# Optimization experiments

Measured on AMD Instinct MI355X. Metric: run time of the kernel, lower is better.

## Reference

```python
import jax, jax.numpy as jnp
import numpy as np

E = 23   # unique_experts_num
K = 3    # act_experts_num
D = 1024 # in_features
H = 768  # hidden_features (0.75 * dim, per MOEBlock mlp_ratio)


def setup_inputs() -> dict:
    key = jax.random.key(0)
    ks = jax.random.split(key, 12)
    s_in = 1.0 / np.sqrt(D)
    s_hid = 1.0 / np.sqrt(H)
    x = jax.random.normal(ks[0], (4, 1024, D), dtype=jnp.float32)
    gate_W = jax.random.normal(ks[1], (D, E), dtype=jnp.float32) * s_in
    gate_b = jnp.zeros((E,), jnp.float32)
    bias = jnp.zeros((E,), jnp.float32)  # registered buffer, init to zeros
    W1 = jax.random.normal(ks[2], (E, D, H), dtype=jnp.float32) * s_in
    b1 = jnp.zeros((E, H), jnp.float32)
    W2 = jax.random.normal(ks[3], (E, H, D), dtype=jnp.float32) * s_hid
    b2 = jnp.zeros((E, D), jnp.float32)
    sW1 = jax.random.normal(ks[4], (D, H), dtype=jnp.float32) * s_in
    sb1 = jnp.zeros((H,), jnp.float32)
    sW2 = jax.random.normal(ks[5], (H, D), dtype=jnp.float32) * s_hid
    sb2 = jnp.zeros((D,), jnp.float32)
    return {"x": x, "gate_W": gate_W, "gate_b": gate_b, "bias": bias,
            "W1": W1, "b1": b1, "W2": W2, "b2": b2,
            "sW1": sW1, "sb1": sb1, "sW2": sW2, "sb2": sb2}


def reference(x, gate_W, gate_b, bias, W1, b1, W2, b2, sW1, sb1, sW2, sb2):
    o_shape = x.shape
    xt = x.reshape(-1, o_shape[-1])          # [T, D]
    T = xt.shape[0]

    # gating: sigmoid gate, top-k indices chosen on (gate + bias), weights gathered from gate
    gate = jax.nn.sigmoid(xt @ gate_W + gate_b)            # [T, E]
    _, top_idx = jax.lax.top_k(gate + bias, K)             # [T, K]
    top_w = jnp.take_along_axis(gate, top_idx, axis=-1)    # [T, K]
    top_w = top_w / jnp.sum(top_w, axis=-1, keepdims=True)

    # combine matrix: C[t, e] = normalized gate weight if e in top-k of token t else 0
    C = jnp.zeros((T, E), xt.dtype).at[jnp.arange(T)[:, None], top_idx].set(top_w)

    # all-expert dense compute (math-equivalent to dispatch/compute/combine)
    h = jax.nn.gelu(jnp.einsum('td,edh->eth', xt, W1) + b1[:, None, :], approximate=False)
    y = jnp.einsum('eth,ehd->etd', h, W2) + b2[:, None, :]  # [E, T, D]
    moe_out = jnp.einsum('etd,te->td', y, C)                # weighted combine

    # shared expert applied to every token
    shared = jax.nn.gelu(xt @ sW1 + sb1, approximate=False) @ sW2 + sb2
    out = shared + moe_out

    # aux load-balance loss
    gate_norm = gate / jnp.sum(gate, axis=-1, keepdims=True)
    P = jnp.mean(gate_norm, axis=0)                          # [E]
    counts = jnp.sum(jax.nn.one_hot(top_idx, E, dtype=jnp.float32), axis=(0, 1))  # [E]
    F = E * counts / (K * T)
    aux_loss = jnp.sum(P * F)

    return out.reshape(o_shape), aux_loss, counts.astype(jnp.int32)
```

## Files before the change

### kernel.cpp

```cpp
#include <hip/hip_runtime.h>
#include <math.h>

#define TT 4096
#define DD 1024
#define HH 768
#define NE 23
#define NG 24
#define BM 128
#define BN 128
#define BK 64
#define MAXT 160
#define KB1 16
#define KB2 12
#define NY1 6
#define NY2 8
#define NWG1 (MAXT*NY1)
#define NWG2 (MAXT*NY2)
#define GATE_BLKS 1024
#define CVT1_BLKS 1152
#define CVT_TOT   2304

#define WS_CURS   0
#define WS_OFFS   576
#define WS_TOTAL  640
#define WS_T2E    672
#define WS_T2A    832
#define WS_TOKE   1024
#define WS_TOKW   13312
#define WS_LTOK   25600
#define WS_LW     41984
#define WS_PPART  58368
#define WS_CPART  81920
#define WS_SIDX   106496
#define XB_OFF  ((size_t)524288)
#define H_OFF   ((size_t)8912896)
#define W1B_OFF ((size_t)34078720)
#define W2B_OFF ((size_t)71827456)

typedef short bf16x8 __attribute__((ext_vector_type(8)));
typedef float f32x4 __attribute__((ext_vector_type(4)));

#define S_BARRIER() asm volatile("s_barrier" ::: "memory")
#define WAIT_VM0()  asm volatile("s_waitcnt vmcnt(0)" ::: "memory")

__device__ inline unsigned short bfr(float f) {
    unsigned u = __float_as_uint(f);
    u += 0x7fffu + ((u >> 16) & 1u);
    return (unsigned short)(u >> 16);
}
__device__ inline unsigned bfr2(float lo, float hi) {
    return (unsigned)bfr(lo) | ((unsigned)bfr(hi) << 16);
}
__device__ inline float b2f(unsigned short u) {
    return __uint_as_float((unsigned)u << 16);
}

__device__ __forceinline__ void gl_lds16(const void* g, void* l) {
    __builtin_amdgcn_global_load_lds(
        (const __attribute__((address_space(1))) unsigned int*)g,
        (__attribute__((address_space(3))) unsigned int*)l, 16, 0, 0);
}

__device__ __forceinline__ void cvt_tile(
    const float* __restrict__ src, unsigned short* __restrict__ dst,
    int N, int KBt, int e, int kb0, int n0, void* smem, int tid)
{
    unsigned (*Ls)[32][65] = (unsigned (*)[32][65])smem;
    const int c = (tid & 15) * 4, r2l = tid >> 4;
    #pragma unroll
    for (int t = 0; t < 2; t++) {
        const float* tsrc = src + (size_t)(kb0 + t) * 64 * N + n0;
        #pragma unroll
        for (int pass = 0; pass < 2; pass++) {
            int row2 = pass * 16 + r2l;
            float4 v0 = *(const float4*)(tsrc + (size_t)(2 * row2) * N + c);
            float4 v1 = *(const float4*)(tsrc + (size_t)(2 * row2 + 1) * N + c);
            uint4 o;
            o.x = bfr2(v0.x, v1.x); o.y = bfr2(v0.y, v1.y);
            o.z = bfr2(v0.z, v1.z); o.w = bfr2(v0.w, v1.w);
            *(uint4*)&Ls[t][row2][c] = o;
        }
    }
    __syncthreads();
    #pragma unroll
    for (int t = 0; t < 2; t++) {
        unsigned short* dbase = dst + ((size_t)(e * KBt + kb0 + t) * N + n0) * 64;
        #pragma unroll
        for (int half = 0; half < 2; half++) {
            int g = half * 256 + tid;
            int n = g >> 3, p = g & 7;
            int j4 = (p ^ (n & 7)) * 4;
            uint4 o;
            o.x = Ls[t][j4 + 0][n]; o.y = Ls[t][j4 + 1][n];
            o.z = Ls[t][j4 + 2][n]; o.w = Ls[t][j4 + 3][n];
            *(uint4*)(dbase + n * 64 + p * 8) = o;
        }
    }
}

__global__ __launch_bounds__(256) void k_gatecvt(
    const float* __restrict__ x, const float* __restrict__ gW,
    const float* __restrict__ gb, const float* __restrict__ bias,
    const float* __restrict__ W1, const float* __restrict__ sW1,
    const float* __restrict__ W2, const float* __restrict__ sW2,
    int* __restrict__ tokE, float* __restrict__ tokW,
    float* __restrict__ Ppart, int* __restrict__ Cpart,
    unsigned short* __restrict__ xb,
    unsigned short* __restrict__ W1b, unsigned short* __restrict__ W2b)
{
    __shared__ __align__(16) char smem[16896];
    const int tid = threadIdx.x;

    if (blockIdx.x >= GATE_BLKS) {
        int id = blockIdx.x - GATE_BLKS;
        if (id < CVT1_BLKS) {
            int n0 = (id % 12) * 64, kb0 = ((id / 12) % 4) * 4, e = id / 48;
            const float* src = (e < NE) ? (W1 + (size_t)e * DD * HH) : sW1;
            cvt_tile(src, W1b, HH, KB1, e, kb0, n0, smem, tid);
            __syncthreads();
            cvt_tile(src, W1b, HH, KB1, e, kb0 + 2, n0, smem, tid);
        } else {
            id -= CVT1_BLKS;
            int n0 = (id % 16) * 64, kb0 = ((id / 16) % 3) * 4, e = id / 48;
            const float* src = (e < NE) ? (W2 + (size_t)e * HH * DD) : sW2;
            cvt_tile(src, W2b, DD, KB2, e, kb0, n0, smem, tid);
            __syncthreads();
            cvt_tile(src, W2b, DD, KB2, e, kb0 + 2, n0, smem, tid);
        }
        return;
    }

    float (*xs)[DD] = (float (*)[DD])smem;
    float (*gv)[NE] = (float (*)[NE])(smem + 16384);
    float* ginvs    = (float*)(smem + 16768);
    int (*sel)[3]   = (int (*)[3])(smem + 16784);
    const int bid = blockIdx.x;
    const int t0 = bid * 4;
    {
        const float4* srcx = (const float4*)(x + (size_t)t0 * DD);
        float4* dstx = (float4*)&xs[0][0];
        #pragma unroll
        for (int i = 0; i < 4; i++) dstx[tid + 256 * i] = srcx[tid + 256 * i];
    }
    __syncthreads();
    {
        const float* xf = &xs[0][0];
        unsigned short* xd = xb + (size_t)t0 * DD;
        #pragma unroll
        for (int it = 0; it < 4; it++) {
            int o = it * 1024 + tid * 4;
            ushort4 u = make_ushort4(bfr(xf[o]), bfr(xf[o + 1]), bfr(xf[o + 2]), bfr(xf[o + 3]));
            *(ushort4*)(xd + o) = u;
        }
    }
    const int w = tid >> 6, l = tid & 63;
    const int t = t0 + w;
    if (l < NE) {
        const float* gc = gW + l;
        const float* xw = xs[w];
        float s[4] = {0.f, 0.f, 0.f, 0.f};
        #pragma unroll 2
        for (int d0 = 0; d0 < DD; d0 += 16) {
            float g[16];
            #pragma unroll
            for (int j = 0; j < 16; j++) g[j] = gc[(d0 + j) * NE];
            #pragma unroll
            for (int j = 0; j < 16; j++) s[j & 3] = fmaf(xw[d0 + j], g[j], s[j & 3]);
        }
        float sv = (s[0] + s[1]) + (s[2] + s[3]) + gb[l];
        gv[w][l] = 1.f / (1.f + expf(-sv));
    }
    __syncthreads();
    if (l == 0) {
        unsigned chosen = 0;
        int be[3]; float bw[3];
        float gsum = 0.f;
        for (int e = 0; e < NE; e++) gsum += gv[w][e];
        #pragma unroll
        for (int k = 0; k < 3; k++) {
            float m = -1e30f; int mi = 0;
            for (int e = 0; e < NE; e++) {
                float kv = gv[w][e] + bias[e];
                if (!((chosen >> e) & 1u) && kv > m) { m = kv; mi = e; }
            }
            chosen |= 1u << mi;
            be[k] = mi; bw[k] = gv[w][mi];
        }
        float inv = 1.f / (bw[0] + bw[1] + bw[2]);
        #pragma unroll
        for (int k = 0; k < 3; k++) {
            tokE[t * 3 + k] = be[k];
            tokW[t * 3 + k] = bw[k] * inv;
            sel[w][k] = be[k];
        }
        ginvs[w] = 1.f / gsum;
    }
    __syncthreads();
    if (tid < NE) {
        float p = gv[0][tid] * ginvs[0] + gv[1][tid] * ginvs[1]
                + gv[2][tid] * ginvs[2] + gv[3][tid] * ginvs[3];
        Ppart[tid * 1024 + bid] = p;
        int c = 0;
        #pragma unroll
        for (int w2 = 0; w2 < 4; w2++)
            #pragma unroll
            for (int k = 0; k < 3; k++) c += (sel[w2][k] == tid);
        Cpart[tid * 1024 + bid] = c;
    }
}

__global__ __launch_bounds__(256) void k_reduce(
    const float* __restrict__ Ppart, const int* __restrict__ Cpart,
    int* __restrict__ counts, float* __restrict__ Psum)
{
    const int e = blockIdx.x;
    const int tid = threadIdx.x;
    float s = 0.f; int c = 0;
    for (int i = tid; i < 1024; i += 256) {
        s += Ppart[e * 1024 + i];
        c += Cpart[e * 1024 + i];
    }
    #pragma unroll
    for (int off = 32; off >= 1; off >>= 1) {
        s += __shfl_down(s, off, 64);
        c += __shfl_down(c, off, 64);
    }
    __shared__ float ss[4]; __shared__ int sc[4];
    if ((tid & 63) == 0) { ss[tid >> 6] = s; sc[tid >> 6] = c; }
    __syncthreads();
    if (tid == 0) {
        Psum[e] = ss[0] + ss[1] + ss[2] + ss[3];
        counts[e] = sc[0] + sc[1] + sc[2] + sc[3];
    }
}

__global__ void k_scan(const int* __restrict__ counts, const float* __restrict__ Psum,
                       int* __restrict__ offs, int* __restrict__ total,
                       int* __restrict__ t2e, int* __restrict__ t2a,
                       int* __restrict__ curs, float* __restrict__ outAux)
{
    const int tid = threadIdx.x;
    for (int i = tid; i < NE * 16; i += 256) curs[i] = 0;
    if (tid != 0) return;
    int off = 0, toff = 0;
    for (int e = 0; e < NG; e++) {
        int c = (e < NE) ? counts[e] : TT;
        offs[e] = off;
        int nt = (c + BM - 1) / BM;
        for (int t = 0; t < nt; t++) {
            t2e[toff + t] = e;
            t2a[toff + t] = off + t * BM;
        }
        off += c; toff += nt;
    }
    offs[NG] = off;
    *total = toff;
    float aux = 0.f;
    for (int e = 0; e < NE; e++) {
        float P = Psum[e] / (float)TT;
        float F = (float)NE * (float)counts[e] / (float)(3 * TT);
        aux += P * F;
    }
    outAux[0] = aux;
    for (int e = 0; e < NE; e++) outAux[1 + e] = (float)counts[e];
}

__global__ void k_scatter(const int* __restrict__ tokE, const float* __restrict__ tokW,
                          const int* __restrict__ offs, int* __restrict__ curs,
                          int* __restrict__ ltok, float* __restrict__ lw,
                          int* __restrict__ sidx)
{
    int t = blockIdx.x * 256 + threadIdx.x;
    if (t >= TT) return;
    #pragma unroll
    for (int k = 0; k < 3; k++) {
        int e = tokE[t * 3 + k];
        int pos = atomicAdd(&curs[e * 16], 1);
        int idx = offs[e] + pos;
        ltok[idx] = t; lw[idx] = tokW[t * 3 + k];
        sidx[t * 3 + k] = idx;
    }
    ltok[3 * TT + t] = t;
    lw[3 * TT + t] = 1.f;
}

__global__ __launch_bounds__(256) void k_mm1(
    const unsigned short* __restrict__ xb, const unsigned short* __restrict__ W1b,
    const float* __restrict__ b1, const float* __restrict__ sb1,
    const int* __restrict__ t2e, const int* __restrict__ t2a,
    const int* __restrict__ offs, const int* __restrict__ total,
    const int* __restrict__ ltok, unsigned short* __restrict__ H)
{
    const int id = blockIdx.x;
    const int wg = (id & 7) * (NWG1 / 8) + (id >> 3);
    const int ns = wg / MAXT;
    const int tb = wg % MAXT;
    if (tb >= *total) return;
    const int e = t2e[tb];
    const int a0 = t2a[tb];
    const int acount = min(offs[e + 1] - a0, BM);
    const float* bb = (e < NE) ? (b1 + e * HH) : sb1;
    const int nb = ns * BN;

    __shared__ unsigned short As[2][BM * BK];
    __shared__ unsigned short Bs[2][BN * BK];
    __shared__ int rows[BM];
    const int tid = threadIdx.x;
    if (tid < BM) rows[tid] = ltok[a0 + min(tid, acount - 1)];
    __syncthreads();

    const int wid = tid >> 6, lane = tid & 63;
    const int wr = wid >> 1, wc = wid & 1;
    const int l15 = lane & 15, l4 = lane >> 4;

    float bv[4];
    #pragma unroll
    for (int n = 0; n < 4; n++) bv[n] = bb[nb + wc * 64 + n * 16 + l15];

    f32x4 acc[4][4];
    #pragma unroll
    for (int m = 0; m < 4; m++)
        #pragma unroll
        for (int n = 0; n < 4; n++) acc[m][n] = (f32x4){0.f, 0.f, 0.f, 0.f};

    const unsigned short* aSrc[4];
    int Goff[4];
    #pragma unroll
    for (int c = 0; c < 4; c++) {
        int G = (wid * 4 + c) * 64 + lane;
        int row = G >> 3, j = G & 7;
        aSrc[c] = xb + (size_t)rows[row] * DD + ((j ^ (row & 7)) << 3);
        Goff[c] = G * 8;
    }
    const unsigned short* wbase = W1b + ((size_t)e * KB1 * HH + nb) * 64;

    auto stage = [&](int buf, int kb) {
        #pragma unroll
        for (int c = 0; c < 4; c++)
            gl_lds16(aSrc[c] + kb * 64, &As[buf][Goff[c]]);
        const unsigned short* wb = wbase + (size_t)kb * (HH * 64);
        #pragma unroll
        for (int c = 0; c < 4; c++)
            gl_lds16(wb + Goff[c], &Bs[buf][Goff[c]]);
    };
    auto compute = [&](int buf) {
        #pragma unroll
        for (int kh = 0; kh < 2; kh++) {
            bf16x8 af[4], bf[4];
            #pragma unroll
            for (int f = 0; f < 4; f++) {
                int ar = wr * 64 + f * 16 + l15;
                int br = wc * 64 + f * 16 + l15;
                int pg = (kh << 2) + l4;
                af[f] = *(const bf16x8*)&As[buf][ar * 64 + ((pg ^ (ar & 7)) << 3)];
                bf[f] = *(const bf16x8*)&Bs[buf][br * 64 + ((pg ^ (br & 7)) << 3)];
            }
            #pragma unroll
            for (int m = 0; m < 4; m++)
                #pragma unroll
                for (int n = 0; n < 4; n++)
                    acc[m][n] = __builtin_amdgcn_mfma_f32_16x16x32_bf16(af[m], bf[n], acc[m][n], 0, 0, 0);
        }
    };

    stage(0, 0);
    WAIT_VM0();
    S_BARRIER();
    int cur = 0;
    #pragma unroll 1
    for (int kb = 0; kb < KB1; kb++) {
        if (kb + 1 < KB1) stage(cur ^ 1, kb + 1);
        __builtin_amdgcn_sched_barrier(0);
        compute(cur);
        if (kb + 1 < KB1) {
            WAIT_VM0();
            S_BARRIER();
            cur ^= 1;
        }
    }

    #pragma unroll
    for (int m = 0; m < 4; m++) {
        int rbase = wr * 64 + m * 16 + l4 * 4;
        #pragma unroll
        for (int n = 0; n < 4; n++) {
            int col = nb + wc * 64 + n * 16 + l15;
            #pragma unroll
            for (int i = 0; i < 4; i++) {
                int r = rbase + i;
                if (r < acount) {
                    float v = acc[m][n][i] + bv[n];
                    float u = v + 0.044715f * v * v * v;
                    float g = v / (1.f + __expf(-1.5957691216f * u));
                    H[(size_t)(a0 + r) * HH + col] = bfr(g);
                }
            }
        }
    }
}

__global__ __launch_bounds__(256) void k_mm2(
    const unsigned short* __restrict__ H, const unsigned short* __restrict__ W2b,
    const float* __restrict__ b2, const float* __restrict__ sb2,
    const int* __restrict__ t2e, const int* __restrict__ t2a,
    const int* __restrict__ offs, const int* __restrict__ total,
    const int* __restrict__ ltok, const float* __restrict__ lw,
    unsigned short* __restrict__ yslot, float* __restrict__ out)
{
    const int id = blockIdx.x;
    const int wg = (id & 7) * (NWG2 / 8) + (id >> 3);
    const int ns = wg / MAXT;
    const int tb = wg % MAXT;
    if (tb >= *total) return;
    const int e = t2e[tb];
    const int a0 = t2a[tb];
    const int acount = min(offs[e + 1] - a0, BM);
    const float* bb = (e < NE) ? (b2 + e * DD) : sb2;
    const int nb = ns * BN;

    __shared__ unsigned short As[2][BM * BK];
    __shared__ unsigned short Bs[2][BN * BK];
    __shared__ int rows[BM];
    __shared__ float wts[BM];
    const int tid = threadIdx.x;
    if (tid < BM) {
        rows[tid] = (tid < acount) ? ltok[a0 + tid] : -1;
        wts[tid]  = (tid < acount) ? lw[a0 + tid] : 0.f;
    }
    __syncthreads();

    const int wid = tid >> 6, lane = tid & 63;
    const int wr = wid >> 1, wc = wid & 1;
    const int l15 = lane & 15, l4 = lane >> 4;

    float bv[4];
    #pragma unroll
    for (int n = 0; n < 4; n++) bv[n] = bb[nb + wc * 64 + n * 16 + l15];

    f32x4 acc[4][4];
    #pragma unroll
    for (int m = 0; m < 4; m++)
        #pragma unroll
        for (int n = 0; n < 4; n++) acc[m][n] = (f32x4){0.f, 0.f, 0.f, 0.f};

    const unsigned short* aSrc[4];
    int Goff[4];
    #pragma unroll
    for (int c = 0; c < 4; c++) {
        int G = (wid * 4 + c) * 64 + lane;
        int row = G >> 3, j = G & 7;
        aSrc[c] = H + (size_t)(a0 + row) * HH + ((j ^ (row & 7)) << 3);
        Goff[c] = G * 8;
    }
    const unsigned short* wbase = W2b + ((size_t)e * KB2 * DD + nb) * 64;

    auto stage = [&](int buf, int kb) {
        #pragma unroll
        for (int c = 0; c < 4; c++)
            gl_lds16(aSrc[c] + kb * 64, &As[buf][Goff[c]]);
        const unsigned short* wb = wbase + (size_t)kb * (DD * 64);
        #pragma unroll
        for (int c = 0; c < 4; c++)
            gl_lds16(wb + Goff[c], &Bs[buf][Goff[c]]);
    };
    auto compute = [&](int buf) {
        #pragma unroll
        for (int kh = 0; kh < 2; kh++) {
            bf16x8 af[4], bf[4];
            #pragma unroll
            for (int f = 0; f < 4; f++) {
                int ar = wr * 64 + f * 16 + l15;
                int br = wc * 64 + f * 16 + l15;
                int pg = (kh << 2) + l4;
                af[f] = *(const bf16x8*)&As[buf][ar * 64 + ((pg ^ (ar & 7)) << 3)];
                bf[f] = *(const bf16x8*)&Bs[buf][br * 64 + ((pg ^ (br & 7)) << 3)];
            }
            #pragma unroll
            for (int m = 0; m < 4; m++)
                #pragma unroll
                for (int n = 0; n < 4; n++)
                    acc[m][n] = __builtin_amdgcn_mfma_f32_16x16x32_bf16(af[m], bf[n], acc[m][n], 0, 0, 0);
        }
    };

    stage(0, 0);
    WAIT_VM0();
    S_BARRIER();
    int cur = 0;
    #pragma unroll 1
    for (int kb = 0; kb < KB2; kb++) {
        if (kb + 1 < KB2) stage(cur ^ 1, kb + 1);
        __builtin_amdgcn_sched_barrier(0);
        compute(cur);
        if (kb + 1 < KB2) {
            WAIT_VM0();
            S_BARRIER();
            cur ^= 1;
        }
    }

    if (e == NE) {
        #pragma unroll
        for (int m = 0; m < 4; m++) {
            int rbase = wr * 64 + m * 16 + l4 * 4;
            #pragma unroll
            for (int n = 0; n < 4; n++) {
                int col = nb + wc * 64 + n * 16 + l15;
                #pragma unroll
                for (int i = 0; i < 4; i++) {
                    int r = rbase + i;
                    out[(size_t)rows[r] * DD + col] = acc[m][n][i] + bv[n];
                }
            }
        }
    } else {
        #pragma unroll
        for (int m = 0; m < 4; m++) {
            int rbase = wr * 64 + m * 16 + l4 * 4;
            #pragma unroll
            for (int n = 0; n < 4; n++) {
                int col = nb + wc * 64 + n * 16 + l15;
                #pragma unroll
                for (int i = 0; i < 4; i++) {
                    int r = rbase + i;
                    if (r < acount)
                        yslot[(size_t)(a0 + r) * DD + col] = bfr(wts[r] * (acc[m][n][i] + bv[n]));
                }
            }
        }
    }
}

__global__ __launch_bounds__(256) void k_combine(
    const unsigned short* __restrict__ yslot, const int* __restrict__ sidx,
    float* __restrict__ out)
{
    const int t = blockIdx.x;
    const int s0 = sidx[t * 3 + 0], s1 = sidx[t * 3 + 1], s2 = sidx[t * 3 + 2];
    const int d = threadIdx.x * 4;
    float* o = out + (size_t)t * DD + d;
    float4 v = *(float4*)o;
    ushort4 a = *(const ushort4*)(yslot + (size_t)s0 * DD + d);
    ushort4 b = *(const ushort4*)(yslot + (size_t)s1 * DD + d);
    ushort4 c = *(const ushort4*)(yslot + (size_t)s2 * DD + d);
    v.x += b2f(a.x) + b2f(b.x) + b2f(c.x);
    v.y += b2f(a.y) + b2f(b.y) + b2f(c.y);
    v.z += b2f(a.z) + b2f(b.z) + b2f(c.z);
    v.w += b2f(a.w) + b2f(b.w) + b2f(c.w);
    *(float4*)o = v;
}

extern "C" void kernel_launch(void* const* d_in, const int* in_sizes, int n_in,
                              void* d_out, int out_size, void* d_ws, size_t ws_size,
                              hipStream_t stream)
{
    const float* x    = (const float*)d_in[0];
    const float* gW   = (const float*)d_in[1];
    const float* gb   = (const float*)d_in[2];
    const float* bias = (const float*)d_in[3];
    const float* W1   = (const float*)d_in[4];
    const float* b1   = (const float*)d_in[5];
    const float* W2   = (const float*)d_in[6];
    const float* b2   = (const float*)d_in[7];
    const float* sW1  = (const float*)d_in[8];
    const float* sb1  = (const float*)d_in[9];
    const float* sW2  = (const float*)d_in[10];
    const float* sb2  = (const float*)d_in[11];
    float* out = (float*)d_out;
    float* wsf = (float*)d_ws;
    int*   wsi = (int*)d_ws;

    int*   curs   = wsi + WS_CURS;
    int*   offs   = wsi + WS_OFFS;
    int*   total  = wsi + WS_TOTAL;
    int*   t2e    = wsi + WS_T2E;
    int*   t2a    = wsi + WS_T2A;
    int*   tokE   = wsi + WS_TOKE;
    float* tokW   = wsf + WS_TOKW;
    int*   ltok   = wsi + WS_LTOK;
    float* lwt    = wsf + WS_LW;
    float* Ppart  = wsf + WS_PPART;
    int*   Cpart  = wsi + WS_CPART;
    int*   sidx   = wsi + WS_SIDX;
    int*   counts = wsi + 432;
    float* Psum   = wsf + 464;
    unsigned short* xb  = (unsigned short*)((char*)d_ws + XB_OFF);
    unsigned short* Hb  = (unsigned short*)((char*)d_ws + H_OFF);
    unsigned short* W1b = (unsigned short*)((char*)d_ws + W1B_OFF);
    unsigned short* W2b = (unsigned short*)((char*)d_ws + W2B_OFF);
    unsigned short* yslot = W1b;

    k_gatecvt<<<GATE_BLKS + CVT_TOT, 256, 0, stream>>>(
        x, gW, gb, bias, W1, sW1, W2, sW2, tokE, tokW, Ppart, Cpart, xb, W1b, W2b);
    k_reduce<<<NE, 256, 0, stream>>>(Ppart, Cpart, counts, Psum);
    k_scan<<<1, 256, 0, stream>>>(counts, Psum, offs, total, t2e, t2a, curs,
                                  out + (size_t)TT * DD);
    k_scatter<<<TT / 256, 256, 0, stream>>>(tokE, tokW, offs, curs, ltok, lwt, sidx);
    k_mm1<<<NWG1, 256, 0, stream>>>(xb, W1b, b1, sb1, t2e, t2a, offs, total, ltok, Hb);
    k_mm2<<<NWG2, 256, 0, stream>>>(Hb, W2b, b2, sb2, t2e, t2a, offs, total, ltok, lwt,
                                    yslot, out);
    k_combine<<<TT, 256, 0, stream>>>(yslot, sidx, out);
}
```

Measured before the change: 212.7 us.

## Split gating from weight conversion and stage gate weights in LDS

The fused gate+convert kernel becomes two launches: a dedicated gating kernel and a weight-conversion kernel. The gating kernel handles 8 tokens per block and first stages the full 1024x23 gate weight matrix in shared memory, padded to 28 columns. Each token is then computed by a 32-lane group doing vectorised LDS reads and a shuffle reduction, where before each lane strided through global memory per expert. This targets the redundant global gate-weight reads, but it uses about 144KB of LDS per block, which limits occupancy, and the gate blocks no longer overlap with conversion work in one grid.

```diff
diff --git a/kernel.cpp b/kernel.cpp
--- a/kernel.cpp
+++ b/kernel.cpp
@@ -16,7 +16,7 @@
 #define NY2 8
 #define NWG1 (MAXT*NY1)
 #define NWG2 (MAXT*NY2)
-#define GATE_BLKS 1024
+#define GATE_BLKS 512
 #define CVT1_BLKS 1152
 #define CVT_TOT   2304
 
@@ -61,6 +61,108 @@
         (__attribute__((address_space(3))) unsigned int*)l, 16, 0, 0);
 }
 
+__global__ __launch_bounds__(256) void k_gate(
+    const float* __restrict__ x, const float* __restrict__ gW,
+    const float* __restrict__ gb, const float* __restrict__ bias,
+    int* __restrict__ tokE, float* __restrict__ tokW,
+    float* __restrict__ Ppart, int* __restrict__ Cpart,
+    unsigned short* __restrict__ xb)
+{
+    __shared__ float gwp[DD * 28];
+    __shared__ float xs[8 * DD];
+    __shared__ float gvv[8][24];
+    __shared__ float ginv[8];
+    __shared__ int   sel[8][3];
+    const int tid = threadIdx.x;
+    const int t0 = blockIdx.x * 8;
+
+    {
+        const float4* sx = (const float4*)(x + (size_t)t0 * DD);
+        float4* dx = (float4*)xs;
+        unsigned short* xd = xb + (size_t)t0 * DD;
+        #pragma unroll
+        for (int c = 0; c < 8; c++) {
+            int idx = c * 256 + tid;
+            float4 v = sx[idx];
+            dx[idx] = v;
+            ushort4 u = make_ushort4(bfr(v.x), bfr(v.y), bfr(v.z), bfr(v.w));
+            *(ushort4*)(xd + idx * 4) = u;
+        }
+    }
+    for (int i = tid; i < DD * NE; i += 256) {
+        int d = i / NE;
+        int e = i - d * NE;
+        gwp[d * 28 + e] = gW[i];
+    }
+    __syncthreads();
+
+    const int t = tid >> 5, s = tid & 31;
+    float acc[24];
+    #pragma unroll
+    for (int e = 0; e < 24; e++) acc[e] = 0.f;
+    const float* xrow = xs + t * DD;
+    #pragma unroll 2
+    for (int j = 0; j < 32; j++) {
+        int d = j * 32 + s;
+        float xv = xrow[d];
+        const float* gr = gwp + d * 28;
+        float g[24];
+        #pragma unroll
+        for (int q = 0; q < 6; q++) {
+            float4 v = *(const float4*)(gr + q * 4);
+            g[4*q] = v.x; g[4*q+1] = v.y; g[4*q+2] = v.z; g[4*q+3] = v.w;
+        }
+        #pragma unroll
+        for (int e = 0; e < 24; e++) acc[e] = fmaf(xv, g[e], acc[e]);
+    }
+    #pragma unroll
+    for (int e = 0; e < 23; e++) {
+        #pragma unroll
+        for (int off = 16; off >= 1; off >>= 1)
+            acc[e] += __shfl_xor(acc[e], off, 32);
+    }
+    __syncthreads();
+    if (s == 0) {
+        float sg[23]; float gsum = 0.f;
+        #pragma unroll
+        for (int e = 0; e < 23; e++) {
+            float sv = 1.f / (1.f + expf(-(acc[e] + gb[e])));
+            sg[e] = sv; gvv[t][e] = sv; gsum += sv;
+        }
+        unsigned chosen = 0; int be[3]; float bw[3];
+        #pragma unroll
+        for (int k = 0; k < 3; k++) {
+            float m = -1e30f; int mi = 0;
+            for (int e = 0; e < 23; e++) {
+                float kv = sg[e] + bias[e];
+                if (!((chosen >> e) & 1u) && kv > m) { m = kv; mi = e; }
+            }
+            chosen |= 1u << mi; be[k] = mi; bw[k] = sg[mi];
+        }
+        float inv = 1.f / (bw[0] + bw[1] + bw[2]);
+        int tt = t0 + t;
+        #pragma unroll
+        for (int k = 0; k < 3; k++) {
+            tokE[tt * 3 + k] = be[k];
+            tokW[tt * 3 + k] = bw[k] * inv;
+            sel[t][k] = be[k];
+        }
+        ginv[t] = 1.f / gsum;
+    }
+    __syncthreads();
+    if (tid < NE) {
+        float p = 0.f; int c = 0;
+        #pragma unroll
+        for (int q = 0; q < 8; q++) {
+            p += gvv[q][tid] * ginv[q];
+            #pragma unroll
+            for (int k = 0; k < 3; k++) c += (sel[q][k] == tid);
+        }
+        Ppart[tid * 1024 + blockIdx.x] = p;
+        Cpart[tid * 1024 + blockIdx.x] = c;
+    }
+}
+
 __device__ __forceinline__ void cvt_tile(
     const float* __restrict__ src, unsigned short* __restrict__ dst,
     int N, int KBt, int e, int kb0, int n0, void* smem, int tid)
@@ -98,114 +200,27 @@
     }
 }
 
-__global__ __launch_bounds__(256) void k_gatecvt(
-    const float* __restrict__ x, const float* __restrict__ gW,
-    const float* __restrict__ gb, const float* __restrict__ bias,
+__global__ __launch_bounds__(256) void k_cvt(
     const float* __restrict__ W1, const float* __restrict__ sW1,
     const float* __restrict__ W2, const float* __restrict__ sW2,
-    int* __restrict__ tokE, float* __restrict__ tokW,
-    float* __restrict__ Ppart, int* __restrict__ Cpart,
-    unsigned short* __restrict__ xb,
     unsigned short* __restrict__ W1b, unsigned short* __restrict__ W2b)
 {
     __shared__ __align__(16) char smem[16896];
     const int tid = threadIdx.x;
-
-    if (blockIdx.x >= GATE_BLKS) {
-        int id = blockIdx.x - GATE_BLKS;
-        if (id < CVT1_BLKS) {
-            int n0 = (id % 12) * 64, kb0 = ((id / 12) % 4) * 4, e = id / 48;
-            const float* src = (e < NE) ? (W1 + (size_t)e * DD * HH) : sW1;
-            cvt_tile(src, W1b, HH, KB1, e, kb0, n0, smem, tid);
-            __syncthreads();
-            cvt_tile(src, W1b, HH, KB1, e, kb0 + 2, n0, smem, tid);
-        } else {
-            id -= CVT1_BLKS;
-            int n0 = (id % 16) * 64, kb0 = ((id / 16) % 3) * 4, e = id / 48;
-            const float* src = (e < NE) ? (W2 + (size_t)e * HH * DD) : sW2;
-            cvt_tile(src, W2b, DD, KB2, e, kb0, n0, smem, tid);
-            __syncthreads();
-            cvt_tile(src, W2b, DD, KB2, e, kb0 + 2, n0, smem, tid);
-        }
-        return;
-    }
-
-    float (*xs)[DD] = (float (*)[DD])smem;
-    float (*gv)[NE] = (float (*)[NE])(smem + 16384);
-    float* ginvs    = (float*)(smem + 16768);
-    int (*sel)[3]   = (int (*)[3])(smem + 16784);
-    const int bid = blockIdx.x;
-    const int t0 = bid * 4;
-    {
-        const float4* srcx = (const float4*)(x + (size_t)t0 * DD);
-        float4* dstx = (float4*)&xs[0][0];
-        #pragma unroll
-        for (int i = 0; i < 4; i++) dstx[tid + 256 * i] = srcx[tid + 256 * i];
-    }
-    __syncthreads();
-    {
-        const float* xf = &xs[0][0];
-        unsigned short* xd = xb + (size_t)t0 * DD;
-        #pragma unroll
-        for (int it = 0; it < 4; it++) {
-            int o = it * 1024 + tid * 4;
-            ushort4 u = make_ushort4(bfr(xf[o]), bfr(xf[o + 1]), bfr(xf[o + 2]), bfr(xf[o + 3]));
-            *(ushort4*)(xd + o) = u;
-        }
-    }
-    const int w = tid >> 6, l = tid & 63;
-    const int t = t0 + w;
-    if (l < NE) {
-        const float* gc = gW + l;
-        const float* xw = xs[w];
-        float s[4] = {0.f, 0.f, 0.f, 0.f};
-        #pragma unroll 2
-        for (int d0 = 0; d0 < DD; d0 += 16) {
-            float g[16];
-            #pragma unroll
-            for (int j = 0; j < 16; j++) g[j] = gc[(d0 + j) * NE];
-            #pragma unroll
-            for (int j = 0; j < 16; j++) s[j & 3] = fmaf(xw[d0 + j], g[j], s[j & 3]);
-        }
-        float sv = (s[0] + s[1]) + (s[2] + s[3]) + gb[l];
-        gv[w][l] = 1.f / (1.f + expf(-sv));
-    }
-    __syncthreads();
-    if (l == 0) {
-        unsigned chosen = 0;
-        int be[3]; float bw[3];
-        float gsum = 0.f;
-        for (int e = 0; e < NE; e++) gsum += gv[w][e];
-        #pragma unroll
-        for (int k = 0; k < 3; k++) {
-            float m = -1e30f; int mi = 0;
-            for (int e = 0; e < NE; e++) {
-                float kv = gv[w][e] + bias[e];
-                if (!((chosen >> e) & 1u) && kv > m) { m = kv; mi = e; }
-            }
-            chosen |= 1u << mi;
-            be[k] = mi; bw[k] = gv[w][mi];
-        }
-        float inv = 1.f / (bw[0] + bw[1] + bw[2]);
-        #pragma unroll
-        for (int k = 0; k < 3; k++) {
-            tokE[t * 3 + k] = be[k];
-            tokW[t * 3 + k] = bw[k] * inv;
-            sel[w][k] = be[k];
-        }
-        ginvs[w] = 1.f / gsum;
-    }
-    __syncthreads();
-    if (tid < NE) {
-        float p = gv[0][tid] * ginvs[0] + gv[1][tid] * ginvs[1]
-                + gv[2][tid] * ginvs[2] + gv[3][tid] * ginvs[3];
-        Ppart[tid * 1024 + bid] = p;
-        int c = 0;
-        #pragma unroll
-        for (int w2 = 0; w2 < 4; w2++)
-            #pragma unroll
-            for (int k = 0; k < 3; k++) c += (sel[w2][k] == tid);
-        Cpart[tid * 1024 + bid] = c;
+    int id = blockIdx.x;
+    if (id < CVT1_BLKS) {
+        int n0 = (id % 12) * 64, kb0 = ((id / 12) % 4) * 4, e = id / 48;
+        const float* src = (e < NE) ? (W1 + (size_t)e * DD * HH) : sW1;
+        cvt_tile(src, W1b, HH, KB1, e, kb0, n0, smem, tid);
+        __syncthreads();
+        cvt_tile(src, W1b, HH, KB1, e, kb0 + 2, n0, smem, tid);
+    } else {
+        id -= CVT1_BLKS;
+        int n0 = (id % 16) * 64, kb0 = ((id / 16) % 3) * 4, e = id / 48;
+        const float* src = (e < NE) ? (W2 + (size_t)e * HH * DD) : sW2;
+        cvt_tile(src, W2b, DD, KB2, e, kb0, n0, smem, tid);
+        __syncthreads();
+        cvt_tile(src, W2b, DD, KB2, e, kb0 + 2, n0, smem, tid);
     }
 }
 
@@ -216,7 +231,7 @@
     const int e = blockIdx.x;
     const int tid = threadIdx.x;
     float s = 0.f; int c = 0;
-    for (int i = tid; i < 1024; i += 256) {
+    for (int i = tid; i < GATE_BLKS; i += 256) {
         s += Ppart[e * 1024 + i];
         c += Cpart[e * 1024 + i];
     }
@@ -590,8 +605,9 @@
     unsigned short* W2b = (unsigned short*)((char*)d_ws + W2B_OFF);
     unsigned short* yslot = W1b;
 
-    k_gatecvt<<<GATE_BLKS + CVT_TOT, 256, 0, stream>>>(
-        x, gW, gb, bias, W1, sW1, W2, sW2, tokE, tokW, Ppart, Cpart, xb, W1b, W2b);
+    k_gate<<<GATE_BLKS, 256, 0, stream>>>(x, gW, gb, bias, tokE, tokW,
+                                          Ppart, Cpart, xb);
+    k_cvt<<<CVT_TOT, 256, 0, stream>>>(W1, sW1, W2, sW2, W1b, W2b);
     k_reduce<<<NE, 256, 0, stream>>>(Ppart, Cpart, counts, Psum);
     k_scan<<<1, 256, 0, stream>>>(counts, Psum, offs, total, t2e, t2a, curs,
                                   out + (size_t)TT * DD);
```

Measured after the change: 218.9 us. +2.9%, slower.
